# Optimization experiments

Hardware: AMD Instinct MI355X
Metric: run time of the kernel (lower is better)

The kernel has to match this reference:

```python
import jax, jax.numpy as jnp
import numpy as np

B, DX, DZ, DY = 8192, 512, 1024, 256


def setup_inputs() -> dict:
    key = jax.random.key(0)
    ks = jax.random.split(key, 13)
    s = 0.02
    return {
        "xs": jax.random.normal(ks[0], (B, DX), dtype=jnp.float32),
        "Wx": jax.random.normal(ks[1], (DZ, DX), dtype=jnp.float32) * s,
        "bx": jnp.zeros((DZ,), dtype=jnp.float32),
        "Wy": jax.random.normal(ks[2], (DZ, DY), dtype=jnp.float32) * s,
        "by": jnp.zeros((DZ,), dtype=jnp.float32),
        "Wn": jax.random.normal(ks[3], (DZ, 3 * DZ), dtype=jnp.float32) * s,
        "bn": jnp.zeros((DZ,), dtype=jnp.float32),
        "Wu": jax.random.normal(ks[4], (DY, DZ), dtype=jnp.float32) * s,
        "bu": jnp.zeros((DY,), dtype=jnp.float32),
        "Wq": jax.random.normal(ks[5], (DY, DZ), dtype=jnp.float32) * s,
        "bq": jnp.zeros((DY,), dtype=jnp.float32),
        "ys_init": jax.random.normal(ks[6], (B, DY), dtype=jnp.float32),
        "zs_init": jax.random.normal(ks[7], (B, DZ), dtype=jnp.float32),
        "T": 4,
        "n": 6,
    }


def reference(xs, Wx, bx, Wy, by, Wn, bn, Wu, bu, Wq, bq, ys_init, zs_init, T, n):
    xs_e = xs @ Wx.T + bx                      # [B, DZ]
    ys_e = ys_init @ Wy.T + by                 # [B, DZ]
    zs = zs_init                               # [B, DZ]
    null = jnp.zeros_like(xs_e)

    def query(x, y, z):
        w = jnp.concatenate([x, y, z], axis=-1)  # [B, 3*DZ]
        return jnp.tanh(w @ Wn.T + bn)

    # no-grad refinement (T-1 outer iterations)
    for _ in range(T - 1):
        for _ in range(n):
            zs = query(xs_e, ys_e, zs)
        ys_e = query(null, ys_e, zs)
    ys_e = jax.lax.stop_gradient(ys_e)
    zs = jax.lax.stop_gradient(zs)

    # final grad-enabled block
    for _ in range(n):
        zs = query(xs_e, ys_e, zs)
    ys_e = query(null, ys_e, zs)

    y_hat = jax.nn.sigmoid(ys_e @ Wu.T + bu)
    q_hat = jax.nn.sigmoid(ys_e @ Wq.T + bq)
    return (y_hat, q_hat)
```

## Files before the change

kernel.cpp:

```cpp
#include <hip/hip_runtime.h>
#include <hip/hip_bf16.h>
#include <cstdint>
#include <cstddef>

#define B_   8192
#define DX_  512
#define DZ_  1024
#define DY_  256
#define T_   4
#define NN_  6

typedef float f32x4 __attribute__((ext_vector_type(4)));
typedef short s16x8 __attribute__((ext_vector_type(8)));
typedef long i64x2 __attribute__((ext_vector_type(2)));
typedef __hip_bfloat16 bf16;

__device__ __forceinline__ void gload_lds16(const void* g, void* l) {
  __builtin_amdgcn_global_load_lds(
      (const __attribute__((address_space(1))) void*)g,
      (__attribute__((address_space(3))) void*)l,
      16, 0, 0);
}

__device__ __forceinline__ float bf2f(unsigned short u) {
  union { unsigned int i; float f; } cv; cv.i = ((unsigned int)u) << 16; return cv.f;
}

__device__ __forceinline__ int permb(int n) {
  return (n & ~63) | (((n >> 3) & 3) << 4) | (((n >> 5) & 1) << 3) | (n & 7);
}

__device__ __forceinline__ void cv4(const float* __restrict__ s, bf16* __restrict__ d, long i) {
  float4 v = ((const float4*)s)[i];
  ushort4 o;
  bf16 a0 = __float2bfloat16(v.x); o.x = *(unsigned short*)&a0;
  bf16 a1 = __float2bfloat16(v.y); o.y = *(unsigned short*)&a1;
  bf16 a2 = __float2bfloat16(v.z); o.z = *(unsigned short*)&a2;
  bf16 a3 = __float2bfloat16(v.w); o.w = *(unsigned short*)&a3;
  ((ushort4*)d)[i] = o;
}
__device__ __forceinline__ void cv4f8(const float* __restrict__ src, unsigned char* __restrict__ dst,
                                      long row, int k0, int srcld, int srcoff) {
  float4 v = *(const float4*)(src + row * srcld + srcoff + k0);
  int p = __builtin_amdgcn_cvt_pk_fp8_f32(v.x, v.y, 0, 0);
  p = __builtin_amdgcn_cvt_pk_fp8_f32(v.z, v.w, p, 1);
  *(int*)(dst + row * DZ_ + permb(k0)) = p;
}

__global__ void cvt_all_kernel(const float* __restrict__ Wn, const float* __restrict__ Wx,
                               const float* __restrict__ Wy, const float* __restrict__ Wu,
                               const float* __restrict__ Wq, const float* __restrict__ xs,
                               const float* __restrict__ ys0, const float* __restrict__ zs0,
                               const float* __restrict__ bu, const float* __restrict__ bq,
                               bf16* __restrict__ Wn_b, bf16* __restrict__ Wx_b,
                               bf16* __restrict__ Wy_b, bf16* __restrict__ Wuq_b,
                               bf16* __restrict__ xs_b, bf16* __restrict__ ysin_b,
                               float* __restrict__ buq,
                               unsigned char* __restrict__ Wnz8, unsigned char* __restrict__ z_a8) {
  const long NWN = (long)DZ_ * 3 * DZ_ / 4, NWX = (long)DZ_ * DX_ / 4,
             NWY = (long)DZ_ * DY_ / 4,     NWU = (long)DY_ * DZ_ / 4,
             NXS = (long)B_ * DX_ / 4,      NYS = (long)B_ * DY_ / 4,
             NBQ = 2 * DY_ / 4,
             NW8 = (long)DZ_ * DZ_ / 4,     NZ8 = (long)B_ * DZ_ / 4;
  const long total = NWN + NWX + NWY + 2 * NWU + NXS + NYS + NBQ + NW8 + NZ8;
  for (long i = (long)blockIdx.x * blockDim.x + threadIdx.x; i < total;
       i += (long)gridDim.x * blockDim.x) {
    long j = i;
    if (j < NWN) { cv4(Wn, Wn_b, j); continue; } j -= NWN;
    if (j < NWX) { cv4(Wx, Wx_b, j); continue; } j -= NWX;
    if (j < NWY) { cv4(Wy, Wy_b, j); continue; } j -= NWY;
    if (j < NWU) { cv4(Wu, Wuq_b, j); continue; } j -= NWU;
    if (j < NWU) { cv4(Wq, Wuq_b + (size_t)DY_ * DZ_, j); continue; } j -= NWU;
    if (j < NXS) { cv4(xs, xs_b, j); continue; } j -= NXS;
    if (j < NYS) { cv4(ys0, ysin_b, j); continue; } j -= NYS;
    if (j < NBQ) {
      float4 v = (j < DY_ / 4) ? ((const float4*)bu)[j] : ((const float4*)bq)[j - DY_ / 4];
      ((float4*)buq)[j] = v; continue;
    } j -= NBQ;
    if (j < NW8) {
      long e = j * 4; long row = e >> 10; int k0 = (int)(e & 1023);
      cv4f8(Wn, Wnz8, row, k0, 3 * DZ_, 2 * DZ_); continue;
    } j -= NW8;
    {
      long e = j * 4; long row = e >> 10; int k0 = (int)(e & 1023);
      cv4f8(zs0, z_a8, row, k0, DZ_, 0);
    }
  }
}

template<int ACT, int MODE, bool HASADD>
__global__ __launch_bounds__(512, 2)
void gemm_bt(const bf16* __restrict__ A, int lda,
             const bf16* __restrict__ W, int ldw,
             const float* __restrict__ bias,
             const bf16* __restrict__ add1,
             bf16* __restrict__ out_pre,
             void* __restrict__ out, void* __restrict__ out2,
             int N, int K)
{
  __shared__ __align__(16) char ldsc[3 * 49152];
  const int t    = threadIdx.x;
  const int lane = t & 63;
  const int wave = t >> 6;
  const int m0 = blockIdx.x * 256;
  const int n0 = blockIdx.y * 128;

  const int srow = t >> 3;
  const int q    = (t & 7) ^ ((t >> 3) & 7);
  const bf16* gA = A + (size_t)(m0 + srow) * lda + q * 8;
  const bf16* gB = W + (size_t)(n0 + srow) * ldw + q * 8;
  const int wb = wave * 1024;

  auto stage = [&](int kt) {
    char* base = ldsc + (kt % 3) * 49152;
    const int ko = kt << 6;
#pragma unroll
    for (int i = 0; i < 4; ++i)
      gload_lds16(gA + (size_t)(i * 64) * lda + ko, base + i * 8192 + wb);
#pragma unroll
    for (int i = 0; i < 2; ++i)
      gload_lds16(gB + (size_t)(i * 64) * ldw + ko, base + 32768 + i * 8192 + wb);
  };

  const int mo = (wave >> 1) * 64;
  const int no = (wave & 1) * 64;
  const int fr = lane & 15;
  const int g4 = lane >> 4;
  const int rb = g4 * 4;

  const int NT = K >> 6;

  float bv[4] = {0.f, 0.f, 0.f, 0.f};
  if (bias) {
#pragma unroll
    for (int j = 0; j < 4; ++j) bv[j] = bias[n0 + no + j * 16 + fr];
  }
  unsigned short adr[4][4][4];
  if (HASADD && MODE != 1) {
#pragma unroll
    for (int f = 0; f < 4; ++f)
#pragma unroll
      for (int j = 0; j < 4; ++j) {
        const unsigned short* p = (const unsigned short*)add1
            + (size_t)(m0 + mo + f * 16 + rb) * N + (n0 + no + j * 16 + fr);
#pragma unroll
        for (int r = 0; r < 4; ++r) adr[f][j][r] = p[(size_t)r * N];
      }
  }
  __builtin_amdgcn_sched_barrier(0);
  stage(0);
  stage(1);
  __builtin_amdgcn_sched_barrier(0);

  f32x4 acc[4][4];
#pragma unroll
  for (int f = 0; f < 4; ++f)
#pragma unroll
    for (int j = 0; j < 4; ++j)
#pragma unroll
      for (int r = 0; r < 4; ++r) {
        float v = bv[j];
        if (HASADD && MODE != 1) v += bf2f(adr[f][j][r]);
        acc[f][j][r] = v;
      }

  s16x8 a0[4], b0[4], a1[4], b1[4];
  auto ldfrags = [&](int kt, int s, s16x8* fa, s16x8* fb) {
    const char* pA = ldsc + (kt % 3) * 49152;
    const char* pB = pA + 32768;
    const int cb = ((s * 4 + g4) ^ (fr & 7)) * 16;
#pragma unroll
    for (int f = 0; f < 4; ++f) fa[f] = *(const s16x8*)(pA + (mo + f * 16 + fr) * 128 + cb);
#pragma unroll
    for (int j = 0; j < 4; ++j) fb[j] = *(const s16x8*)(pB + (no + j * 16 + fr) * 128 + cb);
  };
  auto domfma = [&](const s16x8* fa, const s16x8* fb) {
    __builtin_amdgcn_s_setprio(1);
#pragma unroll
    for (int f = 0; f < 4; ++f)
#pragma unroll
      for (int j = 0; j < 4; ++j)
        acc[f][j] = __builtin_amdgcn_mfma_f32_16x16x32_bf16(fa[f], fb[j], acc[f][j], 0, 0, 0);
    __builtin_amdgcn_s_setprio(0);
  };

  asm volatile("s_waitcnt vmcnt(6)" ::: "memory");
  __builtin_amdgcn_s_barrier();
  __builtin_amdgcn_sched_barrier(0);

  for (int kt = 0; kt < NT; ++kt) {
    ldfrags(kt, 0, a0, b0);
    ldfrags(kt, 1, a1, b1);
    if (kt + 2 < NT) stage(kt + 2);
    __builtin_amdgcn_sched_barrier(0);
    asm volatile("s_waitcnt lgkmcnt(8)" ::: "memory");
    __builtin_amdgcn_sched_barrier(0);
    domfma(a0, b0);
    asm volatile("s_waitcnt lgkmcnt(0)" ::: "memory");
    __builtin_amdgcn_sched_barrier(0);
    domfma(a1, b1);
    if (kt + 2 < NT)      asm volatile("s_waitcnt vmcnt(6)" ::: "memory");
    else if (kt + 1 < NT) asm volatile("s_waitcnt vmcnt(0)" ::: "memory");
    if (kt + 1 < NT) {
      __builtin_amdgcn_s_barrier();
      __builtin_amdgcn_sched_barrier(0);
    }
  }

#pragma unroll
  for (int f = 0; f < 4; ++f) {
#pragma unroll
    for (int j = 0; j < 4; ++j) {
      const int n = n0 + no + j * 16 + fr;
#pragma unroll
      for (int r = 0; r < 4; ++r) {
        const int m = m0 + mo + f * 16 + rb + r;
        float v = acc[f][j][r];
        if (MODE == 1) {
          out_pre[(size_t)m * N + n] = __float2bfloat16(v);
          v += bf2f(((const unsigned short*)add1)[(size_t)m * N + n]);
        }
        if (ACT == 1)      { float e = __expf(2.f * v); v = 1.f - 2.f / (e + 1.f); }
        else if (ACT == 2) v = 1.f / (1.f + __expf(-v));
        if (MODE == 2) {
          if (n < DY_) ((float*)out)[(size_t)m * DY_ + n] = v;
          else         ((float*)out2)[(size_t)m * DY_ + (n - DY_)] = v;
        } else {
          ((bf16*)out)[(size_t)m * N + n] = __float2bfloat16(v);
        }
      }
    }
  }
}

__global__ __launch_bounds__(512, 2)
void gemm_f8(const unsigned char* __restrict__ A8,
             const unsigned char* __restrict__ W8,
             const bf16* __restrict__ add1,
             unsigned char* __restrict__ out8,
             bf16* __restrict__ out16)
{
  __shared__ __align__(16) char ldsc[4 * 24576];
  const int t    = threadIdx.x;
  const int lane = t & 63;
  const int wave = t >> 6;
  const int m0 = blockIdx.x * 256;
  const int n0 = blockIdx.y * 128;

  const int srow = t >> 2;
  const int q    = (t & 3) ^ ((t >> 3) & 3);
  const unsigned char* gA = A8 + (size_t)(m0 + srow) * DZ_ + q * 16;
  const unsigned char* gB = W8 + (size_t)(n0 + srow) * DZ_ + q * 16;
  const int wb = wave * 1024;

  auto stage = [&](int kt) {
    char* base = ldsc + (kt & 3) * 24576;
    const int ko = kt << 6;
    gload_lds16(gA + ko, base + wb);
    gload_lds16(gA + (size_t)128 * DZ_ + ko, base + 8192 + wb);
    gload_lds16(gB + ko, base + 16384 + wb);
  };

  const int mo = (wave >> 1) * 64;
  const int no = (wave & 1) * 64;
  const int fr = lane & 15;
  const int g4 = lane >> 4;
  const int rb = g4 * 4;
  const int cb = (g4 ^ ((fr >> 1) & 3)) * 16;

  const int NT = DZ_ >> 6;

  unsigned short adr[4][4][4];
#pragma unroll
  for (int f = 0; f < 4; ++f)
#pragma unroll
    for (int j = 0; j < 4; ++j) {
      const unsigned short* p = (const unsigned short*)add1
          + (size_t)(m0 + mo + f * 16 + rb) * DZ_ + (n0 + no + j * 16 + fr);
#pragma unroll
      for (int r = 0; r < 4; ++r) adr[f][j][r] = p[(size_t)r * DZ_];
    }
  __builtin_amdgcn_sched_barrier(0);
  stage(0); stage(1); stage(2);
  __builtin_amdgcn_sched_barrier(0);

  f32x4 acc[4][4];
#pragma unroll
  for (int f = 0; f < 4; ++f)
#pragma unroll
    for (int j = 0; j < 4; ++j)
#pragma unroll
      for (int r = 0; r < 4; ++r) acc[f][j][r] = bf2f(adr[f][j][r]);

  asm volatile("s_waitcnt vmcnt(6)" ::: "memory");
  __builtin_amdgcn_s_barrier();
  __builtin_amdgcn_sched_barrier(0);

  for (int kt = 0; kt < NT; ++kt) {
    const char* pA = ldsc + (kt & 3) * 24576;
    const char* pB = pA + 16384;
    i64x2 av[4], bv[4];
#pragma unroll
    for (int f = 0; f < 4; ++f) av[f] = *(const i64x2*)(pA + (mo + f * 16 + fr) * 64 + cb);
#pragma unroll
    for (int j = 0; j < 4; ++j) bv[j] = *(const i64x2*)(pB + (no + j * 16 + fr) * 64 + cb);
    if (kt + 3 < NT) stage(kt + 3);
    __builtin_amdgcn_sched_barrier(0);
    asm volatile("s_waitcnt lgkmcnt(0)" ::: "memory");
    __builtin_amdgcn_sched_barrier(0);
    __builtin_amdgcn_s_setprio(1);
#pragma unroll
    for (int f = 0; f < 4; ++f)
#pragma unroll
      for (int j = 0; j < 4; ++j) {
        acc[f][j] = __builtin_amdgcn_mfma_f32_16x16x32_fp8_fp8(av[f][0], bv[j][0], acc[f][j], 0, 0, 0);
        acc[f][j] = __builtin_amdgcn_mfma_f32_16x16x32_fp8_fp8(av[f][1], bv[j][1], acc[f][j], 0, 0, 0);
      }
    __builtin_amdgcn_s_setprio(0);
    const int rem = NT - 1 - kt;
    if (rem >= 3)      asm volatile("s_waitcnt vmcnt(6)" ::: "memory");
    else if (rem == 2) asm volatile("s_waitcnt vmcnt(3)" ::: "memory");
    else if (rem == 1) asm volatile("s_waitcnt vmcnt(0)" ::: "memory");
    if (rem >= 1) {
      __builtin_amdgcn_s_barrier();
      __builtin_amdgcn_sched_barrier(0);
    }
  }

#pragma unroll
  for (int f = 0; f < 4; ++f) {
#pragma unroll
    for (int j = 0; j < 4; ++j) {
      const int n = n0 + no + j * 16 + fr;
      const int np = permb(n);
#pragma unroll
      for (int r = 0; r < 4; ++r) {
        const int m = m0 + mo + f * 16 + rb + r;
        float v = acc[f][j][r];
        float e = __expf(2.f * v); v = 1.f - 2.f / (e + 1.f);
        if (out8)  out8[(size_t)m * DZ_ + np] =
            (unsigned char)__builtin_amdgcn_cvt_pk_fp8_f32(v, v, 0, 0);
        if (out16) out16[(size_t)m * DZ_ + n] = __float2bfloat16(v);
      }
    }
  }
}

extern "C" void kernel_launch(void* const* d_in, const int* in_sizes, int n_in,
                              void* d_out, int out_size, void* d_ws, size_t ws_size,
                              hipStream_t stream) {
  const float* xs  = (const float*)d_in[0];
  const float* Wx  = (const float*)d_in[1];
  const float* bx  = (const float*)d_in[2];
  const float* Wy  = (const float*)d_in[3];
  const float* by  = (const float*)d_in[4];
  const float* Wn  = (const float*)d_in[5];
  const float* bn  = (const float*)d_in[6];
  const float* Wu  = (const float*)d_in[7];
  const float* bu  = (const float*)d_in[8];
  const float* Wq  = (const float*)d_in[9];
  const float* bq  = (const float*)d_in[10];
  const float* ys0 = (const float*)d_in[11];
  const float* zs0 = (const float*)d_in[12];

  char* ws = (char*)d_ws;
  size_t off = 0;
  auto take = [&](size_t bytes) -> char* {
    char* p = ws + off;
    off += (bytes + 255) & ~(size_t)255;
    return p;
  };

  bf16*  Wn_b   = (bf16*)take((size_t)DZ_ * 3 * DZ_ * 2);
  bf16*  Wx_b   = (bf16*)take((size_t)DZ_ * DX_ * 2);
  bf16*  Wy_b   = (bf16*)take((size_t)DZ_ * DY_ * 2);
  bf16*  Wuq_b  = (bf16*)take((size_t)2 * DY_ * DZ_ * 2);
  float* buq    = (float*)take((size_t)2 * DY_ * 4);
  bf16*  ys_b   = (bf16*)take((size_t)B_ * DZ_ * 2);
  bf16*  z_a    = (bf16*)take((size_t)B_ * DZ_ * 2);
  bf16*  z_b    = (bf16*)take((size_t)B_ * DZ_ * 2);
  bf16*  cx     = (bf16*)take((size_t)B_ * DZ_ * 2);
  bf16*  cy     = (bf16*)take((size_t)B_ * DZ_ * 2);
  bf16*  c      = (bf16*)take((size_t)B_ * DZ_ * 2);
  unsigned char* Wnz8 = (unsigned char*)take((size_t)DZ_ * DZ_);
  unsigned char* z_a8 = (unsigned char*)take((size_t)B_ * DZ_);
  unsigned char* z_b8 = (unsigned char*)take((size_t)B_ * DZ_);
  bf16* xs_b   = c;
  bf16* ysin_b = (bf16*)((char*)c + (size_t)B_ * DX_ * 2);
  bf16* xse_b  = cy;

  cvt_all_kernel<<<2048, 256, 0, stream>>>(Wn, Wx, Wy, Wu, Wq, xs, ys0, zs0, bu, bq,
                                           Wn_b, Wx_b, Wy_b, Wuq_b,
                                           xs_b, ysin_b, buq, Wnz8, z_a8);

  const dim3 blk(512);
  const dim3 gz(B_ / 256, DZ_ / 128);
  const dim3 gh(B_ / 256, 4);

  gemm_bt<0, 0, false><<<gz, blk, 0, stream>>>(xs_b, DX_, Wx_b, DX_, bx, nullptr, nullptr, xse_b, nullptr, DZ_, DX_);
  gemm_bt<0, 0, false><<<gz, blk, 0, stream>>>(ysin_b, DY_, Wy_b, DY_, by, nullptr, nullptr, ys_b, nullptr, DZ_, DY_);
  gemm_bt<0, 0, false><<<gz, blk, 0, stream>>>(xse_b, DZ_, Wn_b, 3 * DZ_, nullptr, nullptr, nullptr, cx, nullptr, DZ_, DZ_);

  unsigned char* zc8 = z_a8;
  unsigned char* zn8 = z_b8;
  for (int tt = 0; tt < T_; ++tt) {
    gemm_bt<0, 1, true><<<gz, blk, 0, stream>>>(ys_b, DZ_, Wn_b + DZ_, 3 * DZ_, bn, cx, cy, c, nullptr, DZ_, DZ_);
    if (tt < T_ - 1) {
      for (int i = 0; i < NN_; ++i) {
        bf16* shadow = (tt == T_ - 2 && i == NN_ - 1) ? z_a : nullptr;
        gemm_f8<<<gz, blk, 0, stream>>>(zc8, Wnz8, c, zn8, shadow);
        unsigned char* t8 = zc8; zc8 = zn8; zn8 = t8;
      }
      gemm_f8<<<gz, blk, 0, stream>>>(zc8, Wnz8, cy, nullptr, ys_b);
    } else {
      bf16* zc = z_a;
      bf16* zn = z_b;
      for (int i = 0; i < NN_; ++i) {
        gemm_bt<1, 0, true><<<gz, blk, 0, stream>>>(zc, DZ_, Wn_b + 2 * DZ_, 3 * DZ_, nullptr, c, nullptr, zn, nullptr, DZ_, DZ_);
        bf16* tmp = zc; zc = zn; zn = tmp;
      }
      gemm_bt<1, 0, true><<<gz, blk, 0, stream>>>(zc, DZ_, Wn_b + 2 * DZ_, 3 * DZ_, nullptr, cy, nullptr, ys_b, nullptr, DZ_, DZ_);
    }
  }

  float* outp = (float*)d_out;
  gemm_bt<2, 2, false><<<gh, blk, 0, stream>>>(ys_b, DZ_, Wuq_b, DZ_, buq, nullptr, nullptr,
                                               outp, outp + (size_t)B_ * DY_, 2 * DY_, DZ_);
}
```

Baseline: 813.8 us.

## Switch fp8 GEMM to 16x16x128 scaled MFMA with 128-wide K tiles

Replaces the pair of 16x16x32 fp8 MFMAs per K-step with the gfx950 mfma_scale 16x16x128 f8f6f4 instruction, using unit scales. K tiles widen from 64 to 128 bytes, LDS stages go from four to three buffers of 48KB, and the swizzle is redone for the 128-byte rows. The permuted fp8 layout is dropped so operands are stored in natural order. This aims to cut MFMA issue count and loop overhead per K step; the larger LDS footprint and shallower prefetch may reduce latency hiding.

Result: slower. 3.164 ms (+288.8%).

```diff
diff --git a/kernel.cpp b/kernel.cpp
--- a/kernel.cpp
+++ b/kernel.cpp
@@ -12,7 +12,8 @@
 
 typedef float f32x4 __attribute__((ext_vector_type(4)));
 typedef short s16x8 __attribute__((ext_vector_type(8)));
-typedef long i64x2 __attribute__((ext_vector_type(2)));
+typedef int   i32x4 __attribute__((ext_vector_type(4)));
+typedef int   i32x8 __attribute__((ext_vector_type(8)));
 typedef __hip_bfloat16 bf16;
 
 __device__ __forceinline__ void gload_lds16(const void* g, void* l) {
@@ -24,10 +25,6 @@
 
 __device__ __forceinline__ float bf2f(unsigned short u) {
   union { unsigned int i; float f; } cv; cv.i = ((unsigned int)u) << 16; return cv.f;
-}
-
-__device__ __forceinline__ int permb(int n) {
-  return (n & ~63) | (((n >> 3) & 3) << 4) | (((n >> 5) & 1) << 3) | (n & 7);
 }
 
 __device__ __forceinline__ void cv4(const float* __restrict__ s, bf16* __restrict__ d, long i) {
@@ -44,7 +41,7 @@
   float4 v = *(const float4*)(src + row * srcld + srcoff + k0);
   int p = __builtin_amdgcn_cvt_pk_fp8_f32(v.x, v.y, 0, 0);
   p = __builtin_amdgcn_cvt_pk_fp8_f32(v.z, v.w, p, 1);
-  *(int*)(dst + row * DZ_ + permb(k0)) = p;
+  *(int*)(dst + row * DZ_ + k0) = p;
 }
 
 __global__ void cvt_all_kernel(const float* __restrict__ Wn, const float* __restrict__ Wx,
@@ -233,6 +230,12 @@
   }
 }
 
+__device__ __forceinline__ i32x8 ld8(const char* rp, int p0, int p1) {
+  i32x4 lo = *(const i32x4*)(rp + p0);
+  i32x4 hi = *(const i32x4*)(rp + p1);
+  return __builtin_shufflevector(lo, hi, 0, 1, 2, 3, 4, 5, 6, 7);
+}
+
 __global__ __launch_bounds__(512, 2)
 void gemm_f8(const unsigned char* __restrict__ A8,
              const unsigned char* __restrict__ W8,
@@ -240,25 +243,28 @@
              unsigned char* __restrict__ out8,
              bf16* __restrict__ out16)
 {
-  __shared__ __align__(16) char ldsc[4 * 24576];
+  __shared__ __align__(16) char ldsc[3 * 49152];
   const int t    = threadIdx.x;
   const int lane = t & 63;
   const int wave = t >> 6;
   const int m0 = blockIdx.x * 256;
   const int n0 = blockIdx.y * 128;
 
-  const int srow = t >> 2;
-  const int q    = (t & 3) ^ ((t >> 3) & 3);
-  const unsigned char* gA = A8 + (size_t)(m0 + srow) * DZ_ + q * 16;
-  const unsigned char* gB = W8 + (size_t)(n0 + srow) * DZ_ + q * 16;
+  const int srow = t >> 3;
+  const int q8   = (t & 7) ^ ((t >> 3) & 7);
+  const unsigned char* gA = A8 + (size_t)(m0 + srow) * DZ_ + q8 * 16;
+  const unsigned char* gB = W8 + (size_t)(n0 + srow) * DZ_ + q8 * 16;
   const int wb = wave * 1024;
 
   auto stage = [&](int kt) {
-    char* base = ldsc + (kt & 3) * 24576;
-    const int ko = kt << 6;
-    gload_lds16(gA + ko, base + wb);
-    gload_lds16(gA + (size_t)128 * DZ_ + ko, base + 8192 + wb);
-    gload_lds16(gB + ko, base + 16384 + wb);
+    char* base = ldsc + (kt % 3) * 49152;
+    const int ko = kt << 7;
+#pragma unroll
+    for (int i = 0; i < 4; ++i)
+      gload_lds16(gA + (size_t)(i * 64) * DZ_ + ko, base + i * 8192 + wb);
+#pragma unroll
+    for (int i = 0; i < 2; ++i)
+      gload_lds16(gB + (size_t)(i * 64) * DZ_ + ko, base + 32768 + i * 8192 + wb);
   };
 
   const int mo = (wave >> 1) * 64;
@@ -266,9 +272,10 @@
   const int fr = lane & 15;
   const int g4 = lane >> 4;
   const int rb = g4 * 4;
-  const int cb = (g4 ^ ((fr >> 1) & 3)) * 16;
-
-  const int NT = DZ_ >> 6;
+  const int p0 = (((g4 << 1) ^ (fr & 7)) << 4);
+  const int p1 = p0 ^ 16;
+
+  const int NT = DZ_ >> 7;
 
   unsigned short adr[4][4][4];
 #pragma unroll
@@ -281,7 +288,7 @@
       for (int r = 0; r < 4; ++r) adr[f][j][r] = p[(size_t)r * DZ_];
     }
   __builtin_amdgcn_sched_barrier(0);
-  stage(0); stage(1); stage(2);
+  stage(0); stage(1);
   __builtin_amdgcn_sched_barrier(0);
 
   f32x4 acc[4][4];
@@ -297,31 +304,28 @@
   __builtin_amdgcn_sched_barrier(0);
 
   for (int kt = 0; kt < NT; ++kt) {
-    const char* pA = ldsc + (kt & 3) * 24576;
-    const char* pB = pA + 16384;
-    i64x2 av[4], bv[4];
-#pragma unroll
-    for (int f = 0; f < 4; ++f) av[f] = *(const i64x2*)(pA + (mo + f * 16 + fr) * 64 + cb);
-#pragma unroll
-    for (int j = 0; j < 4; ++j) bv[j] = *(const i64x2*)(pB + (no + j * 16 + fr) * 64 + cb);
-    if (kt + 3 < NT) stage(kt + 3);
-    __builtin_amdgcn_sched_barrier(0);
+    const char* pA = ldsc + (kt % 3) * 49152;
+    const char* pB = pA + 32768;
+    i32x8 bv[4];
+#pragma unroll
+    for (int j = 0; j < 4; ++j)
+      bv[j] = ld8(pB + (no + j * 16 + fr) * 128, p0, p1);
+    if (kt + 2 < NT) stage(kt + 2);
+    __builtin_amdgcn_s_setprio(1);
+#pragma unroll
+    for (int f = 0; f < 4; ++f) {
+      i32x8 a = ld8(pA + (mo + f * 16 + fr) * 128, p0, p1);
+#pragma unroll
+      for (int j = 0; j < 4; ++j)
+        acc[f][j] = __builtin_amdgcn_mfma_scale_f32_16x16x128_f8f6f4(
+            a, bv[j], acc[f][j], 0, 0, 0, 0x7f7f7f7f, 0, 0x7f7f7f7f);
+    }
+    __builtin_amdgcn_s_setprio(0);
     asm volatile("s_waitcnt lgkmcnt(0)" ::: "memory");
     __builtin_amdgcn_sched_barrier(0);
-    __builtin_amdgcn_s_setprio(1);
-#pragma unroll
-    for (int f = 0; f < 4; ++f)
-#pragma unroll
-      for (int j = 0; j < 4; ++j) {
-        acc[f][j] = __builtin_amdgcn_mfma_f32_16x16x32_fp8_fp8(av[f][0], bv[j][0], acc[f][j], 0, 0, 0);
-        acc[f][j] = __builtin_amdgcn_mfma_f32_16x16x32_fp8_fp8(av[f][1], bv[j][1], acc[f][j], 0, 0, 0);
-      }
-    __builtin_amdgcn_s_setprio(0);
-    const int rem = NT - 1 - kt;
-    if (rem >= 3)      asm volatile("s_waitcnt vmcnt(6)" ::: "memory");
-    else if (rem == 2) asm volatile("s_waitcnt vmcnt(3)" ::: "memory");
-    else if (rem == 1) asm volatile("s_waitcnt vmcnt(0)" ::: "memory");
-    if (rem >= 1) {
+    if (kt + 2 < NT)      asm volatile("s_waitcnt vmcnt(6)" ::: "memory");
+    else if (kt + 1 < NT) asm volatile("s_waitcnt vmcnt(0)" ::: "memory");
+    if (kt + 1 < NT) {
       __builtin_amdgcn_s_barrier();
       __builtin_amdgcn_sched_barrier(0);
     }
@@ -332,13 +336,12 @@
 #pragma unroll
     for (int j = 0; j < 4; ++j) {
       const int n = n0 + no + j * 16 + fr;
-      const int np = permb(n);
 #pragma unroll
       for (int r = 0; r < 4; ++r) {
         const int m = m0 + mo + f * 16 + rb + r;
         float v = acc[f][j][r];
         float e = __expf(2.f * v); v = 1.f - 2.f / (e + 1.f);
-        if (out8)  out8[(size_t)m * DZ_ + np] =
+        if (out8)  out8[(size_t)m * DZ_ + n] =
             (unsigned char)__builtin_amdgcn_cvt_pk_fp8_f32(v, v, 0, 0);
         if (out16) out16[(size_t)m * DZ_ + n] = __float2bfloat16(v);
       }
```
